# Performance work log

Measured on AMD Instinct MI355X. Metric: run time of the kernel, lower is better.

The kernel has to match this reference:

```python
import jax, jax.numpy as jnp
import numpy as np

B, H, W, C, G = 4, 56, 56, 256, 16
K = 9  # 3x3 deformable kernel
GC = C // G


def _ln(x, g, b, eps=1e-5):
    mu = jnp.mean(x, axis=-1, keepdims=True)
    var = jnp.mean(jnp.square(x - mu), axis=-1, keepdims=True)
    return (x - mu) * jax.lax.rsqrt(var + eps) * g + b


def _gelu(x):
    return jax.nn.gelu(x, approximate=False)  # torch nn.GELU default = exact erf


def _dcnv3_core(x, offset, mask):
    # x: [B,H,W,C]; offset: [B,H,W,G*K*2] (x,y per point); mask: [B,H,W,G,K] softmaxed over K
    xg = x.reshape(B, H * W, G, GC)
    off = offset.reshape(B, H, W, G, K, 2)
    dy, dx = jnp.meshgrid(jnp.arange(-1.0, 2.0), jnp.arange(-1.0, 2.0), indexing="ij")
    dx = dx.reshape(K).astype(x.dtype)
    dy = dy.reshape(K).astype(x.dtype)
    gx = jnp.arange(W, dtype=x.dtype)[None, None, :, None, None]
    gy = jnp.arange(H, dtype=x.dtype)[None, :, None, None, None]
    # sampling locations in unpadded pixel coords (zeros outside image == F.pad + zero grid_sample)
    px = gx + dx + off[..., 0]  # [B,H,W,G,K]
    py = gy + dy + off[..., 1]

    def flat(p):  # [B,H,W,G,K] -> [B, H*W*K, G]
        return p.transpose(0, 1, 2, 4, 3).reshape(B, H * W * K, G)

    pxf, pyf = flat(px), flat(py)
    x0 = jnp.floor(pxf)
    y0 = jnp.floor(pyf)
    acc = jnp.zeros((B, H * W * K, G, GC), x.dtype)
    for cx, cy in ((x0, y0), (x0 + 1, y0), (x0, y0 + 1), (x0 + 1, y0 + 1)):
        wgt = (1 - jnp.abs(pxf - cx)) * (1 - jnp.abs(pyf - cy))
        valid = ((cx >= 0) & (cx < W) & (cy >= 0) & (cy < H)).astype(x.dtype)
        idx = (jnp.clip(cy, 0, H - 1).astype(jnp.int32) * W
               + jnp.clip(cx, 0, W - 1).astype(jnp.int32))[..., None]  # [B,HWK,G,1]
        v = jnp.take_along_axis(xg, idx, axis=1)  # [B,HWK,G,GC]
        acc = acc + (wgt * valid)[..., None] * v
    mf = flat(mask)[..., None]  # [B,HWK,G,1]
    out = (acc * mf).reshape(B, H * W, K, G, GC).sum(axis=2)
    return out.reshape(B, H, W, C)


def _dcn(x, w_in, b_in, w_dw, b_dw, ln_dw_g, ln_dw_b, w_off, b_off,
         w_mask, b_mask, w_out, b_out):
    xp = x @ w_in + b_in  # input projection (value branch)
    x1 = jax.lax.conv_general_dilated(
        x, w_dw, window_strides=(1, 1), padding="SAME",
        dimension_numbers=("NHWC", "HWIO", "NHWC"), feature_group_count=C) + b_dw
    x1 = _gelu(_ln(x1, ln_dw_g, ln_dw_b))  # dw_conv -> LN -> GELU
    offset = x1 @ w_off + b_off  # [B,H,W,G*K*2]
    mask = jax.nn.softmax((x1 @ w_mask + b_mask).reshape(B, H, W, G, K), axis=-1)
    y = _dcnv3_core(xp, offset, mask)
    return y @ w_out + b_out


def _block(x, w_in, b_in, w_dw, b_dw, ln_dw_g, ln_dw_b, w_off, b_off,
           w_mask, b_mask, w_out, b_out, ln1_g, ln1_b,
           w_fc1, b_fc1, w_fc2, b_fc2, ln2_g, ln2_b, gamma1, gamma2):
    # post_norm=True: x = x + gamma1*LN1(dcn(x)); x = x + gamma2*LN2(mlp(x))
    y = _dcn(x, w_in, b_in, w_dw, b_dw, ln_dw_g, ln_dw_b, w_off, b_off,
             w_mask, b_mask, w_out, b_out)
    x = x + gamma1 * _ln(y, ln1_g, ln1_b)
    m = _gelu(x @ w_fc1 + b_fc1) @ w_fc2 + b_fc2  # MLP (dropout = identity)
    x = x + gamma2 * _ln(m, ln2_g, ln2_b)
    return x


def setup_inputs() -> dict:
    key = jax.random.key(0)
    ks = jax.random.split(key, 9)
    f = jnp.float32

    def rn(k, shape, s=0.02):
        return jax.random.normal(k, shape, dtype=f) * s

    return {
        "x": jax.random.normal(ks[0], (B, H, W, C), dtype=f),
        "w_in": rn(ks[1], (C, C)), "b_in": jnp.zeros((C,), f),
        "w_dw": rn(ks[2], (3, 3, 1, C), 0.1), "b_dw": jnp.zeros((C,), f),
        "ln_dw_g": jnp.ones((C,), f), "ln_dw_b": jnp.zeros((C,), f),
        "w_off": rn(ks[3], (C, G * K * 2)), "b_off": jnp.zeros((G * K * 2,), f),
        "w_mask": rn(ks[4], (C, G * K)), "b_mask": jnp.zeros((G * K,), f),
        "w_out": rn(ks[5], (C, C)), "b_out": jnp.zeros((C,), f),
        "ln1_g": jnp.ones((C,), f), "ln1_b": jnp.zeros((C,), f),
        "w_fc1": rn(ks[6], (C, C)), "b_fc1": jnp.zeros((C,), f),
        "w_fc2": rn(ks[7], (C, C)), "b_fc2": jnp.zeros((C,), f),
        "ln2_g": jnp.ones((C,), f), "ln2_b": jnp.zeros((C,), f),
        "gamma1": jnp.ones((C,), f), "gamma2": jnp.ones((C,), f),
    }


def reference(x, w_in, b_in, w_dw, b_dw, ln_dw_g, ln_dw_b, w_off, b_off,
              w_mask, b_mask, w_out, b_out, ln1_g, ln1_b,
              w_fc1, b_fc1, w_fc2, b_fc2, ln2_g, ln2_b, gamma1, gamma2):
    return _block(x, w_in, b_in, w_dw, b_dw, ln_dw_g, ln_dw_b, w_off, b_off,
                  w_mask, b_mask, w_out, b_out, ln1_g, ln1_b,
                  w_fc1, b_fc1, w_fc2, b_fc2, ln2_g, ln2_b, gamma1, gamma2)
```

## Files before the change

### kernel.cpp

```cpp
#include <hip/hip_runtime.h>
#include <math.h>

typedef unsigned short u16;
typedef unsigned int u32;
typedef __attribute__((ext_vector_type(8))) short short8;
typedef __attribute__((ext_vector_type(4))) float f32x4;

#define NB 4
#define NH 56
#define NW 56
#define HW2 (NH*NW)
#define NPIX (NB*HW2)

__device__ __forceinline__ u16 f2b(float f) {
  union { float f; u32 u; } a; a.f = f;
  return (u16)((a.u + 0x7FFFu + ((a.u >> 16) & 1u)) >> 16);
}
__device__ __forceinline__ float b2f(u16 v) {
  union { u32 u; float f; } a; a.u = ((u32)v) << 16; return a.f;
}
__device__ __forceinline__ float gelu_exact(float v) {
  return 0.5f * v * (1.0f + erff(v * 0.70710678118654752f));
}
__device__ __forceinline__ int xcd_swz(int bid, int nwg) {
  const int q = nwg >> 3, r = nwg & 7, x = bid & 7, j = bid >> 3;
  return (x < r ? x * (q + 1) : r * (q + 1) + (x - r) * q) + j;
}
__device__ __forceinline__ u32 swz(int r, int b) {
  return (u32)(r * 512 + ((b ^ (r & 7)) << 4));
}

__global__ __launch_bounds__(256) void k1_kernel(
    const float* __restrict__ w_in, const float* __restrict__ w_out,
    const float* __restrict__ w_fc1, const float* __restrict__ w_fc2,
    const float* __restrict__ w_off, const float* __restrict__ w_mask,
    const float* __restrict__ b_off, const float* __restrict__ b_mask,
    u16* __restrict__ wT, float* __restrict__ bias_cat,
    const float* __restrict__ xf, const float* __restrict__ wdw,
    const float* __restrict__ bdw, const float* __restrict__ lng,
    const float* __restrict__ lnb, u16* __restrict__ x1)
{
  const int blk = blockIdx.x, t = threadIdx.x;
  if (blk < 1456) {
    const float* src; int n, N;
    if      (blk < 256)  { src = w_in;   n = blk;        N = 256; }
    else if (blk < 512)  { src = w_out;  n = blk - 256;  N = 256; }
    else if (blk < 768)  { src = w_fc1;  n = blk - 512;  N = 256; }
    else if (blk < 1024) { src = w_fc2;  n = blk - 768;  N = 256; }
    else if (blk < 1312) { src = w_off;  n = blk - 1024; N = 288; }
    else                 { src = w_mask; n = blk - 1312; N = 144; }
    wT[blk * 256 + t] = f2b(src[t * N + n]);
  } else if (blk == 1456) {
    for (int j = t; j < 432; j += 256)
      bias_cat[j] = (j < 288) ? b_off[j] : b_mask[j - 288];
  } else {
    const int pb = xcd_swz(blk - 1457, 3136);
    const int p = pb * 4 + (t >> 6);
    const int lane = t & 63, c0 = lane * 4;
    const int bb = p / HW2, hw = p - bb * HW2;
    const int h = hw / NW, w = hw - h * NW;
    float4 bd = *(const float4*)(bdw + c0);
    float a0 = bd.x, a1 = bd.y, a2 = bd.z, a3 = bd.w;
    #pragma unroll
    for (int kh = 0; kh < 3; ++kh) {
      const int hh = h + kh - 1;
      if ((unsigned)hh >= NH) continue;
      #pragma unroll
      for (int kw = 0; kw < 3; ++kw) {
        const int ww = w + kw - 1;
        if ((unsigned)ww >= NW) continue;
        float4 v = *(const float4*)(xf + (size_t)(bb * HW2 + hh * NW + ww) * 256 + c0);
        float4 wv = *(const float4*)(wdw + (kh * 3 + kw) * 256 + c0);
        a0 += v.x * wv.x; a1 += v.y * wv.y;
        a2 += v.z * wv.z; a3 += v.w * wv.w;
      }
    }
    float s1 = a0 + a1 + a2 + a3;
    float s2 = a0 * a0 + a1 * a1 + a2 * a2 + a3 * a3;
    #pragma unroll
    for (int d = 1; d < 64; d <<= 1) { s1 += __shfl_xor(s1, d); s2 += __shfl_xor(s2, d); }
    const float mu = s1 * (1.0f / 256.0f);
    const float var = s2 * (1.0f / 256.0f) - mu * mu;
    const float rs = rsqrtf(var + 1e-5f);
    float4 lg4 = *(const float4*)(lng + c0);
    float4 lb4 = *(const float4*)(lnb + c0);
    ushort4 o;
    o.x = f2b(gelu_exact((a0 - mu) * rs * lg4.x + lb4.x));
    o.y = f2b(gelu_exact((a1 - mu) * rs * lg4.y + lb4.y));
    o.z = f2b(gelu_exact((a2 - mu) * rs * lg4.z + lb4.z));
    o.w = f2b(gelu_exact((a3 - mu) * rs * lg4.w + lb4.w));
    *(ushort4*)(x1 + (size_t)p * 256 + c0) = o;
  }
}

template<int AF32>
__device__ __forceinline__ void gemm64_body(
    const void* __restrict__ Asrc, const u16* __restrict__ Brows,
    const float* __restrict__ bias, u16* __restrict__ Cout,
    int Ntot, int m0, int n0, char* As, char* Bs, int t)
{
  if (AF32) {
    const int r = t >> 2;
    const float4* src = (const float4*)((const float*)Asrc + (size_t)(m0 + r) * 256);
    #pragma unroll
    for (int i = 0; i < 16; ++i) {
      const int f4 = (t & 3) + i * 4;
      float4 v = src[f4];
      uint2 pk;
      pk.x = (u32)f2b(v.x) | ((u32)f2b(v.y) << 16);
      pk.y = (u32)f2b(v.z) | ((u32)f2b(v.w) << 16);
      *(uint2*)(As + swz(r, f4 >> 1) + (f4 & 1) * 8) = pk;
    }
  } else {
    const int r = t >> 2, c0 = t & 3;
    const u16* Ag = (const u16*)Asrc + (size_t)(m0 + r) * 256;
    #pragma unroll
    for (int i = 0; i < 8; ++i) {
      const int b = c0 + i * 4;
      *(uint4*)(As + swz(r, b)) = *(const uint4*)(Ag + b * 8);
    }
  }
  {
    const int r = t >> 2, c0 = t & 3;
    const int nrow = n0 + r;
    const u16* Bg = Brows + (size_t)nrow * 256;
    const bool bok = nrow < Ntot;
    #pragma unroll
    for (int i = 0; i < 8; ++i) {
      const int b = c0 + i * 4;
      uint4 bv = make_uint4(0u, 0u, 0u, 0u);
      if (bok) bv = *(const uint4*)(Bg + b * 8);
      *(uint4*)(Bs + swz(r, b)) = bv;
    }
  }
  __syncthreads();
  const int l = t & 63, w = t >> 6;
  const int wm = (w >> 1) << 5, wn = (w & 1) << 5;
  const int lr = l & 15, lk = l >> 4;
  const int ra0 = wm + lr, ra1 = wm + 16 + lr;
  const int rb0 = wn + lr, rb1 = wn + 16 + lr;
  f32x4 acc00 = {}, acc01 = {}, acc10 = {}, acc11 = {};
  #pragma unroll
  for (int ks = 0; ks < 8; ++ks) {
    const int bb = ks * 4 + lk;
    short8 a0 = *(const short8*)(As + swz(ra0, bb));
    short8 a1 = *(const short8*)(As + swz(ra1, bb));
    short8 b0 = *(const short8*)(Bs + swz(rb0, bb));
    short8 b1 = *(const short8*)(Bs + swz(rb1, bb));
    acc00 = __builtin_amdgcn_mfma_f32_16x16x32_bf16(a0, b0, acc00, 0, 0, 0);
    acc01 = __builtin_amdgcn_mfma_f32_16x16x32_bf16(a0, b1, acc01, 0, 0, 0);
    acc10 = __builtin_amdgcn_mfma_f32_16x16x32_bf16(a1, b0, acc10, 0, 0, 0);
    acc11 = __builtin_amdgcn_mfma_f32_16x16x32_bf16(a1, b1, acc11, 0, 0, 0);
  }
  const f32x4 accs[2][2] = {{acc00, acc01}, {acc10, acc11}};
  #pragma unroll
  for (int mi = 0; mi < 2; ++mi)
    #pragma unroll
    for (int ni = 0; ni < 2; ++ni) {
      const int col = n0 + wn + ni * 16 + lr;
      if (col < Ntot) {
        const float bv = bias[col];
        #pragma unroll
        for (int r4 = 0; r4 < 4; ++r4) {
          const int row = m0 + wm + mi * 16 + lk * 4 + r4;
          Cout[(size_t)row * Ntot + col] = f2b(accs[mi][ni][r4] + bv);
        }
      }
    }
}

__global__ __launch_bounds__(256) void k2_kernel(
    const float* __restrict__ xf, const u16* __restrict__ x1,
    const u16* __restrict__ wT, const float* __restrict__ b_in,
    const float* __restrict__ bcat, u16* __restrict__ xp_bf,
    u16* __restrict__ omb)
{
  __shared__ u16 lds[32768];
  char* As = (char*)lds;
  char* Bs = (char*)(lds + 16384);
  const int t = threadIdx.x;
  if (blockIdx.x < 784) {
    const int sb = xcd_swz(blockIdx.x, 784);
    const int m0 = (sb >> 2) * 64, n0 = (sb & 3) * 64;
    gemm64_body<1>(xf, wT, b_in, xp_bf, 256, m0, n0, As, Bs, t);
  } else {
    const int sb = xcd_swz((int)blockIdx.x - 784, 1372);
    const int m0 = (sb / 7) * 64, n0 = (sb % 7) * 64;
    gemm64_body<0>(x1, wT + 1024 * 256, bcat, omb, 432, m0, n0, As, Bs, t);
  }
}

__global__ __launch_bounds__(256) void dcnv3_kernel(
    const u16* __restrict__ xp, const u16* __restrict__ omb,
    u16* __restrict__ y)
{
  __shared__ u16 lom[8 * 432];
  const int sb = xcd_swz(blockIdx.x, NPIX / 8);
  const int p0 = sb * 8;
  for (int i = threadIdx.x; i < 432; i += 256) {
    const int row = i / 54, u = i - row * 54;
    *(uint4*)(lom + row * 432 + u * 8) =
        *(const uint4*)(omb + (size_t)(p0 + row) * 432 + u * 8);
  }
  __syncthreads();
  const int tid = threadIdx.x;
  const int lp = tid >> 5, gh = tid & 31;
  const int g = gh >> 1, hf = gh & 1;
  const int p = p0 + lp;
  const int bb = p / HW2, hw = p - bb * HW2;
  const int h = hw / NW, w = hw - h * NW;
  const u16* off = lom + lp * 432 + g * 18;
  const u16* mk  = lom + lp * 432 + 288 + g * 9;
  float lg[9];
  float mx = -1e30f;
  #pragma unroll
  for (int k = 0; k < 9; ++k) { lg[k] = b2f(mk[k]); mx = fmaxf(mx, lg[k]); }
  float se = 0.0f;
  #pragma unroll
  for (int k = 0; k < 9; ++k) { lg[k] = __expf(lg[k] - mx); se += lg[k]; }
  const float inv = 1.0f / se;

  float a[8] = {0.f,0.f,0.f,0.f,0.f,0.f,0.f,0.f};
  const u16* base = xp + ((size_t)bb * HW2) * 256 + g * 16 + hf * 8;
  #pragma unroll
  for (int k = 0; k < 9; ++k) {
    const float px = (float)(w + (k % 3) - 1) + b2f(off[2 * k]);
    const float py = (float)(h + (k / 3) - 1) + b2f(off[2 * k + 1]);
    const float fx = floorf(px), fy = floorf(py);
    const int ix = (int)fx, iy = (int)fy;
    const float ax = px - fx, ay = py - fy;
    const float mwt = lg[k] * inv;
    const float w00 = (1.0f - ax) * (1.0f - ay) * mwt;
    const float w10 = ax * (1.0f - ay) * mwt;
    const float w01 = (1.0f - ax) * ay * mwt;
    const float w11 = ax * ay * mwt;
    auto corner = [&](int cx, int cy, float wt) {
      if (cx < 0 || cx >= NW || cy < 0 || cy >= NH) return;
      uint4 v = *(const uint4*)(base + (size_t)(cy * NW + cx) * 256);
      const u32 wv[4] = {v.x, v.y, v.z, v.w};
      #pragma unroll
      for (int j = 0; j < 4; ++j) {
        union { u32 u; float f; } lo, hi;
        lo.u = wv[j] << 16; hi.u = wv[j] & 0xffff0000u;
        a[2 * j]     += wt * lo.f;
        a[2 * j + 1] += wt * hi.f;
      }
    };
    corner(ix,     iy,     w00);
    corner(ix + 1, iy,     w10);
    corner(ix,     iy + 1, w01);
    corner(ix + 1, iy + 1, w11);
  }
  u16 tmp[8];
  #pragma unroll
  for (int j = 0; j < 8; ++j) tmp[j] = f2b(a[j]);
  *(uint4*)(y + ((size_t)p * 256 + g * 16 + hf * 8)) = *(const uint4*)(tmp);
}

__global__ __launch_bounds__(512) void mega3_kernel(
    const u16* __restrict__ ybf, const u16* __restrict__ wT,
    const float* __restrict__ x, const float* __restrict__ b_out,
    const float* __restrict__ gamma1, const float* __restrict__ ln1g,
    const float* __restrict__ ln1b, const float* __restrict__ b_fc1,
    const float* __restrict__ b_fc2, const float* __restrict__ gamma2,
    const float* __restrict__ ln2g, const float* __restrict__ ln2b,
    float* __restrict__ out)
{
  __shared__ u16 As[64 * 256];
  __shared__ float redS[64][4], redQ[64][4];
  const int t = threadIdx.x;
  const int m0 = blockIdx.x * 64;
  const int l = t & 63, w = t >> 6;
  const int wm = w >> 2, wn = w & 3;
  const int lr = l & 15, lk = l >> 4;
  const int ra0 = wm * 32 + lr, ra1 = wm * 32 + 16 + lr;
  const int colb = wn * 64 + lr;

  {
    const int r = t >> 3, j0 = (t & 7) * 4;
    const uint4* src = (const uint4*)(ybf + (size_t)(m0 + r) * 256);
    #pragma unroll
    for (int i = 0; i < 4; ++i)
      *(uint4*)((char*)As + swz(r, j0 + i)) = src[j0 + i];
  }
  __syncthreads();

  f32x4 acc[2][4];
  auto do_gemm = [&](const u16* Bt) {
    #pragma unroll
    for (int mi = 0; mi < 2; ++mi)
      #pragma unroll
      for (int ni = 0; ni < 4; ++ni) acc[mi][ni] = (f32x4){0.f,0.f,0.f,0.f};
    const u16* Bbase = Bt + (size_t)(wn * 64 + lr) * 256 + lk * 8;
    #pragma unroll
    for (int ks = 0; ks < 8; ++ks) {
      short8 a0 = *(const short8*)((char*)As + swz(ra0, ks * 4 + lk));
      short8 a1 = *(const short8*)((char*)As + swz(ra1, ks * 4 + lk));
      #pragma unroll
      for (int ni = 0; ni < 4; ++ni) {
        short8 b = *(const short8*)(Bbase + ni * 16 * 256 + ks * 32);
        acc[0][ni] = __builtin_amdgcn_mfma_f32_16x16x32_bf16(a0, b, acc[0][ni], 0, 0, 0);
        acc[1][ni] = __builtin_amdgcn_mfma_f32_16x16x32_bf16(a1, b, acc[1][ni], 0, 0, 0);
      }
    }
  };
  auto lds_write_b16 = [&](int row, int col, u16 v) {
    *(u16*)((char*)As + row * 512 + (((col >> 3) ^ (row & 7)) << 4) + (col & 7) * 2) = v;
  };
  auto ln_reduce = [&](const float bv[4], float s1[2][4], float s2[2][4]) {
    #pragma unroll
    for (int mi = 0; mi < 2; ++mi)
      #pragma unroll
      for (int r4 = 0; r4 < 4; ++r4) {
        float s = 0.f, q = 0.f;
        #pragma unroll
        for (int ni = 0; ni < 4; ++ni) {
          const float v = acc[mi][ni][r4] + bv[ni];
          s += v; q += v * v;
        }
        s1[mi][r4] = s; s2[mi][r4] = q;
      }
    #pragma unroll
    for (int d = 1; d < 16; d <<= 1)
      #pragma unroll
      for (int mi = 0; mi < 2; ++mi)
        #pragma unroll
        for (int r4 = 0; r4 < 4; ++r4) {
          s1[mi][r4] += __shfl_xor(s1[mi][r4], d);
          s2[mi][r4] += __shfl_xor(s2[mi][r4], d);
        }
    if (lr == 0) {
      #pragma unroll
      for (int mi = 0; mi < 2; ++mi)
        #pragma unroll
        for (int r4 = 0; r4 < 4; ++r4) {
          const int rl = wm * 32 + mi * 16 + lk * 4 + r4;
          redS[rl][wn] = s1[mi][r4];
          redQ[rl][wn] = s2[mi][r4];
        }
    }
    __syncthreads();
  };

  do_gemm(wT + 256 * 256);
  float bv1[4], s1[2][4], s2[2][4];
  #pragma unroll
  for (int ni = 0; ni < 4; ++ni) bv1[ni] = b_out[colb + ni * 16];
  ln_reduce(bv1, s1, s2);

  float x2r[2][4][4];
  {
    float gmv[4], lgv[4], lbv[4];
    #pragma unroll
    for (int ni = 0; ni < 4; ++ni) {
      gmv[ni] = gamma1[colb + ni * 16];
      lgv[ni] = ln1g[colb + ni * 16];
      lbv[ni] = ln1b[colb + ni * 16];
    }
    #pragma unroll
    for (int mi = 0; mi < 2; ++mi)
      #pragma unroll
      for (int r4 = 0; r4 < 4; ++r4) {
        const int rl = wm * 32 + mi * 16 + lk * 4 + r4;
        const float S = redS[rl][0] + redS[rl][1] + redS[rl][2] + redS[rl][3];
        const float Q = redQ[rl][0] + redQ[rl][1] + redQ[rl][2] + redQ[rl][3];
        const float mu = S * (1.0f / 256.0f);
        const float var = Q * (1.0f / 256.0f) - mu * mu;
        const float rs = rsqrtf(var + 1e-5f);
        const int row = m0 + rl;
        #pragma unroll
        for (int ni = 0; ni < 4; ++ni) {
          const float v = acc[mi][ni][r4] + bv1[ni];
          const float o = x[(size_t)row * 256 + colb + ni * 16]
                        + gmv[ni] * ((v - mu) * rs * lgv[ni] + lbv[ni]);
          x2r[mi][r4][ni] = o;
          lds_write_b16(rl, colb + ni * 16, f2b(o));
        }
      }
  }
  __syncthreads();

  do_gemm(wT + 512 * 256);
  float m1v[2][4][4];
  #pragma unroll
  for (int mi = 0; mi < 2; ++mi)
    #pragma unroll
    for (int r4 = 0; r4 < 4; ++r4)
      #pragma unroll
      for (int ni = 0; ni < 4; ++ni)
        m1v[mi][r4][ni] = gelu_exact(acc[mi][ni][r4] + b_fc1[colb + ni * 16]);
  __syncthreads();
  #pragma unroll
  for (int mi = 0; mi < 2; ++mi)
    #pragma unroll
    for (int r4 = 0; r4 < 4; ++r4) {
      const int rl = wm * 32 + mi * 16 + lk * 4 + r4;
      #pragma unroll
      for (int ni = 0; ni < 4; ++ni)
        lds_write_b16(rl, colb + ni * 16, f2b(m1v[mi][r4][ni]));
    }
  __syncthreads();

  do_gemm(wT + 768 * 256);
  float bv3[4];
  #pragma unroll
  for (int ni = 0; ni < 4; ++ni) bv3[ni] = b_fc2[colb + ni * 16];
  ln_reduce(bv3, s1, s2);
  {
    float gmv[4], lgv[4], lbv[4];
    #pragma unroll
    for (int ni = 0; ni < 4; ++ni) {
      gmv[ni] = gamma2[colb + ni * 16];
      lgv[ni] = ln2g[colb + ni * 16];
      lbv[ni] = ln2b[colb + ni * 16];
    }
    #pragma unroll
    for (int mi = 0; mi < 2; ++mi)
      #pragma unroll
      for (int r4 = 0; r4 < 4; ++r4) {
        const int rl = wm * 32 + mi * 16 + lk * 4 + r4;
        const float S = redS[rl][0] + redS[rl][1] + redS[rl][2] + redS[rl][3];
        const float Q = redQ[rl][0] + redQ[rl][1] + redQ[rl][2] + redQ[rl][3];
        const float mu = S * (1.0f / 256.0f);
        const float var = Q * (1.0f / 256.0f) - mu * mu;
        const float rs = rsqrtf(var + 1e-5f);
        const int row = m0 + rl;
        #pragma unroll
        for (int ni = 0; ni < 4; ++ni) {
          const float v = acc[mi][ni][r4] + bv3[ni];
          out[(size_t)row * 256 + colb + ni * 16] =
              x2r[mi][r4][ni] + gmv[ni] * ((v - mu) * rs * lgv[ni] + lbv[ni]);
        }
      }
  }
}

static constexpr size_t OFF_WT  = 0;
static constexpr size_t OFF_BC  = 745472;
static constexpr size_t OFF_XP  = 747520;
static constexpr size_t OFF_X1  = 7170048;
static constexpr size_t OFF_OMB = 13592576;
static constexpr size_t OFF_Y   = 24430592;

extern "C" void kernel_launch(void* const* d_in, const int* in_sizes, int n_in,
                              void* d_out, int out_size, void* d_ws, size_t ws_size,
                              hipStream_t stream)
{
  const float* x      = (const float*)d_in[0];
  const float* w_in   = (const float*)d_in[1];
  const float* b_in   = (const float*)d_in[2];
  const float* w_dw   = (const float*)d_in[3];
  const float* b_dw   = (const float*)d_in[4];
  const float* ln_dw_g= (const float*)d_in[5];
  const float* ln_dw_b= (const float*)d_in[6];
  const float* w_off  = (const float*)d_in[7];
  const float* b_off  = (const float*)d_in[8];
  const float* w_mask = (const float*)d_in[9];
  const float* b_mask = (const float*)d_in[10];
  const float* w_out  = (const float*)d_in[11];
  const float* b_out  = (const float*)d_in[12];
  const float* ln1_g  = (const float*)d_in[13];
  const float* ln1_b  = (const float*)d_in[14];
  const float* w_fc1  = (const float*)d_in[15];
  const float* b_fc1  = (const float*)d_in[16];
  const float* w_fc2  = (const float*)d_in[17];
  const float* b_fc2  = (const float*)d_in[18];
  const float* ln2_g  = (const float*)d_in[19];
  const float* ln2_b  = (const float*)d_in[20];
  const float* gamma1 = (const float*)d_in[21];
  const float* gamma2 = (const float*)d_in[22];
  float* out = (float*)d_out;

  char* ws = (char*)d_ws;
  u16*   wT    = (u16*)  (ws + OFF_WT);
  float* bcat  = (float*)(ws + OFF_BC);
  u16*   xp_bf = (u16*)  (ws + OFF_XP);
  u16*   x1    = (u16*)  (ws + OFF_X1);
  u16*   omb   = (u16*)  (ws + OFF_OMB);
  u16*   ybf   = (u16*)  (ws + OFF_Y);

  k1_kernel<<<dim3(1457 + 3136), 256, 0, stream>>>(
      w_in, w_out, w_fc1, w_fc2, w_off, w_mask, b_off, b_mask, wT, bcat,
      x, w_dw, b_dw, ln_dw_g, ln_dw_b, x1);
  k2_kernel<<<dim3(784 + 1372), 256, 0, stream>>>(
      x, x1, wT, b_in, bcat, xp_bf, omb);
  dcnv3_kernel<<<dim3(NPIX / 8), 256, 0, stream>>>(xp_bf, omb, ybf);
  mega3_kernel<<<dim3(196), 512, 0, stream>>>(
      ybf, wT, x, b_out, gamma1, ln1_g, ln1_b, b_fc1, b_fc2,
      gamma2, ln2_g, ln2_b, out);
}
```

Before: 93.46 us.

## Stage neighborhood tile of xp in LDS for deformable sampling

The DCNv3 sampling kernel now cooperatively loads a 5x12 pixel window of the value projection (all 256 channels) into shared memory around each block's 8 pixels. Bilinear corner fetches whose sample falls inside that window read from LDS, and the rest fall back to global memory. This is meant to cut repeated scattered global or L2 gathers, since neighbouring output pixels hit overlapping input texels. In exchange it adds about 30KB of LDS per block, which can lower occupancy, adds an upfront tile load that may fetch unused data, and introduces a divergent branch. It also assumes the 8 pixels of a block lie in one image row (56 is divisible by 8).

```diff
diff --git a/kernel.cpp b/kernel.cpp
--- a/kernel.cpp
+++ b/kernel.cpp
@@ -195,20 +195,32 @@
     u16* __restrict__ y)
 {
   __shared__ u16 lom[8 * 432];
+  __shared__ u16 ltile[5 * 12 * 256];
   const int sb = xcd_swz(blockIdx.x, NPIX / 8);
   const int p0 = sb * 8;
+  const int bb = p0 / HW2, hw0 = p0 - bb * HW2;
+  const int h = hw0 / NW, w0 = hw0 - h * NW;
+  const u16* xb = xp + (size_t)bb * HW2 * 256;
   for (int i = threadIdx.x; i < 432; i += 256) {
     const int row = i / 54, u = i - row * 54;
     *(uint4*)(lom + row * 432 + u * 8) =
         *(const uint4*)(omb + (size_t)(p0 + row) * 432 + u * 8);
   }
+  for (int i = threadIdx.x; i < 1920; i += 256) {
+    const int texel = i >> 5, part = i & 31;
+    const int ly = texel / 12, lx = texel - ly * 12;
+    const int gy = h - 2 + ly, gx = w0 - 2 + lx;
+    if ((unsigned)gy < NH && (unsigned)gx < NW)
+      *(uint4*)(ltile + texel * 256 + part * 8) =
+          *(const uint4*)(xb + (size_t)(gy * NW + gx) * 256 + part * 8);
+  }
   __syncthreads();
+
   const int tid = threadIdx.x;
   const int lp = tid >> 5, gh = tid & 31;
   const int g = gh >> 1, hf = gh & 1;
-  const int p = p0 + lp;
-  const int bb = p / HW2, hw = p - bb * HW2;
-  const int h = hw / NW, w = hw - h * NW;
+  const int w = w0 + lp;
+  const int choff = g * 16 + hf * 8;
   const u16* off = lom + lp * 432 + g * 18;
   const u16* mk  = lom + lp * 432 + 288 + g * 9;
   float lg[9];
@@ -221,7 +233,17 @@
   const float inv = 1.0f / se;
 
   float a[8] = {0.f,0.f,0.f,0.f,0.f,0.f,0.f,0.f};
-  const u16* base = xp + ((size_t)bb * HW2) * 256 + g * 16 + hf * 8;
+  const u16* gbase = xb + choff;
+  auto fma8 = [&](uint4 v, float wt) {
+    const u32 wv[4] = {v.x, v.y, v.z, v.w};
+    #pragma unroll
+    for (int j = 0; j < 4; ++j) {
+      union { u32 u; float f; } lo, hi;
+      lo.u = wv[j] << 16; hi.u = wv[j] & 0xffff0000u;
+      a[2 * j]     += wt * lo.f;
+      a[2 * j + 1] += wt * hi.f;
+    }
+  };
   #pragma unroll
   for (int k = 0; k < 9; ++k) {
     const float px = (float)(w + (k % 3) - 1) + b2f(off[2 * k]);
@@ -234,27 +256,32 @@
     const float w10 = ax * (1.0f - ay) * mwt;
     const float w01 = (1.0f - ax) * ay * mwt;
     const float w11 = ax * ay * mwt;
-    auto corner = [&](int cx, int cy, float wt) {
-      if (cx < 0 || cx >= NW || cy < 0 || cy >= NH) return;
-      uint4 v = *(const uint4*)(base + (size_t)(cy * NW + cx) * 256);
-      const u32 wv[4] = {v.x, v.y, v.z, v.w};
-      #pragma unroll
-      for (int j = 0; j < 4; ++j) {
-        union { u32 u; float f; } lo, hi;
-        lo.u = wv[j] << 16; hi.u = wv[j] & 0xffff0000u;
-        a[2 * j]     += wt * lo.f;
-        a[2 * j + 1] += wt * hi.f;
-      }
-    };
-    corner(ix,     iy,     w00);
-    corner(ix + 1, iy,     w10);
-    corner(ix,     iy + 1, w01);
-    corner(ix + 1, iy + 1, w11);
+    const bool inw = (ix >= w0 - 2) && (ix <= w0 + 8) && (iy >= h - 2) && (iy <= h + 1);
+    if (inw) {
+      auto cornerL = [&](int cx, int cy, float wt) {
+        if (cx < 0 || cx >= NW || cy < 0 || cy >= NH) return;
+        const u16* vp = ltile + (((cy - (h - 2)) * 12 + (cx - (w0 - 2))) << 8) + choff;
+        fma8(*(const uint4*)vp, wt);
+      };
+      cornerL(ix,     iy,     w00);
+      cornerL(ix + 1, iy,     w10);
+      cornerL(ix,     iy + 1, w01);
+      cornerL(ix + 1, iy + 1, w11);
+    } else {
+      auto cornerG = [&](int cx, int cy, float wt) {
+        if (cx < 0 || cx >= NW || cy < 0 || cy >= NH) return;
+        fma8(*(const uint4*)(gbase + (size_t)(cy * NW + cx) * 256), wt);
+      };
+      cornerG(ix,     iy,     w00);
+      cornerG(ix + 1, iy,     w10);
+      cornerG(ix,     iy + 1, w01);
+      cornerG(ix + 1, iy + 1, w11);
+    }
   }
   u16 tmp[8];
   #pragma unroll
   for (int j = 0; j < 8; ++j) tmp[j] = f2b(a[j]);
-  *(uint4*)(y + ((size_t)p * 256 + g * 16 + hf * 8)) = *(const uint4*)(tmp);
+  *(uint4*)(y + ((size_t)(p0 + lp) * 256 + choff)) = *(const uint4*)(tmp);
 }
 
 __global__ __launch_bounds__(512) void mega3_kernel(
```

Result: no change. 94.48 us (+1.1%).

## Fuse DCNv3 sampling into the output-projection/MLP tail kernel

Applied to the files above, without the earlier changes.

Merges the deformable sampling kernel into the tail GEMM+LayerNorm+MLP kernel. Each 512-thread block now handles 32 pixels, writing the sampled output straight into swizzled LDS instead of round-tripping a bf16 buffer through global memory. This also removes one kernel launch. In exchange, the tail GEMMs use 32-row tiles with 8 waves splitting N, so each loaded weight is reused less. The sampling phase also has fewer threads per pixel (16 instead of 32), each doing twice the work.

```diff
diff --git a/kernel.cpp b/kernel.cpp
--- a/kernel.cpp
+++ b/kernel.cpp
@@ -190,114 +190,100 @@
   }
 }
 
-__global__ __launch_bounds__(256) void dcnv3_kernel(
+__global__ __launch_bounds__(512) void dcn_tail_kernel(
     const u16* __restrict__ xp, const u16* __restrict__ omb,
-    u16* __restrict__ y)
+    const u16* __restrict__ wT, const float* __restrict__ x,
+    const float* __restrict__ b_out, const float* __restrict__ gamma1,
+    const float* __restrict__ ln1g, const float* __restrict__ ln1b,
+    const float* __restrict__ b_fc1, const float* __restrict__ b_fc2,
+    const float* __restrict__ gamma2, const float* __restrict__ ln2g,
+    const float* __restrict__ ln2b, float* __restrict__ out)
 {
-  __shared__ u16 lom[8 * 432];
-  const int sb = xcd_swz(blockIdx.x, NPIX / 8);
-  const int p0 = sb * 8;
-  for (int i = threadIdx.x; i < 432; i += 256) {
+  __shared__ u16 As[32 * 256];
+  __shared__ u16 lom[32 * 432];
+  __shared__ float redS[32][8], redQ[32][8];
+  const int t = threadIdx.x;
+  const int blk = xcd_swz(blockIdx.x, 392);
+  const int p0 = blk * 32;
+
+  for (int i = t; i < 1728; i += 512) {
     const int row = i / 54, u = i - row * 54;
     *(uint4*)(lom + row * 432 + u * 8) =
         *(const uint4*)(omb + (size_t)(p0 + row) * 432 + u * 8);
   }
   __syncthreads();
-  const int tid = threadIdx.x;
-  const int lp = tid >> 5, gh = tid & 31;
-  const int g = gh >> 1, hf = gh & 1;
-  const int p = p0 + lp;
-  const int bb = p / HW2, hw = p - bb * HW2;
-  const int h = hw / NW, w = hw - h * NW;
-  const u16* off = lom + lp * 432 + g * 18;
-  const u16* mk  = lom + lp * 432 + 288 + g * 9;
-  float lg[9];
-  float mx = -1e30f;
-  #pragma unroll
-  for (int k = 0; k < 9; ++k) { lg[k] = b2f(mk[k]); mx = fmaxf(mx, lg[k]); }
-  float se = 0.0f;
-  #pragma unroll
-  for (int k = 0; k < 9; ++k) { lg[k] = __expf(lg[k] - mx); se += lg[k]; }
-  const float inv = 1.0f / se;
-
-  float a[8] = {0.f,0.f,0.f,0.f,0.f,0.f,0.f,0.f};
-  const u16* base = xp + ((size_t)bb * HW2) * 256 + g * 16 + hf * 8;
-  #pragma unroll
-  for (int k = 0; k < 9; ++k) {
-    const float px = (float)(w + (k % 3) - 1) + b2f(off[2 * k]);
-    const float py = (float)(h + (k / 3) - 1) + b2f(off[2 * k + 1]);
-    const float fx = floorf(px), fy = floorf(py);
-    const int ix = (int)fx, iy = (int)fy;
-    const float ax = px - fx, ay = py - fy;
-    const float mwt = lg[k] * inv;
-    const float w00 = (1.0f - ax) * (1.0f - ay) * mwt;
-    const float w10 = ax * (1.0f - ay) * mwt;
-    const float w01 = (1.0f - ax) * ay * mwt;
-    const float w11 = ax * ay * mwt;
+
+  {
+    const int lp = t >> 4, g = t & 15;
+    const int p = p0 + lp;
+    const int bb = p / HW2, hw = p - bb * HW2;
+    const int h = hw / NW, w = hw - h * NW;
+    const u16* off = lom + lp * 432 + g * 18;
+    const u16* mk  = lom + lp * 432 + 288 + g * 9;
+    float lg[9];
+    float mx = -1e30f;
+    #pragma unroll
+    for (int k = 0; k < 9; ++k) { lg[k] = b2f(mk[k]); mx = fmaxf(mx, lg[k]); }
+    float se = 0.0f;
+    #pragma unroll
+    for (int k = 0; k < 9; ++k) { lg[k] = __expf(lg[k] - mx); se += lg[k]; }
+    const float inv = 1.0f / se;
+    float a[16];
+    #pragma unroll
+    for (int j = 0; j < 16; ++j) a[j] = 0.f;
+    const u16* gbase = xp + (size_t)bb * HW2 * 256 + g * 16;
     auto corner = [&](int cx, int cy, float wt) {
       if (cx < 0 || cx >= NW || cy < 0 || cy >= NH) return;
-      uint4 v = *(const uint4*)(base + (size_t)(cy * NW + cx) * 256);
-      const u32 wv[4] = {v.x, v.y, v.z, v.w};
-      #pragma unroll
-      for (int j = 0; j < 4; ++j) {
+      const u16* vp = gbase + (size_t)(cy * NW + cx) * 256;
+      uint4 v0 = *(const uint4*)vp;
+      uint4 v1 = *(const uint4*)(vp + 8);
+      const u32 wv[8] = {v0.x, v0.y, v0.z, v0.w, v1.x, v1.y, v1.z, v1.w};
+      #pragma unroll
+      for (int j = 0; j < 8; ++j) {
         union { u32 u; float f; } lo, hi;
         lo.u = wv[j] << 16; hi.u = wv[j] & 0xffff0000u;
         a[2 * j]     += wt * lo.f;
         a[2 * j + 1] += wt * hi.f;
       }
     };
-    corner(ix,     iy,     w00);
-    corner(ix + 1, iy,     w10);
-    corner(ix,     iy + 1, w01);
-    corner(ix + 1, iy + 1, w11);
-  }
-  u16 tmp[8];
-  #pragma unroll
-  for (int j = 0; j < 8; ++j) tmp[j] = f2b(a[j]);
-  *(uint4*)(y + ((size_t)p * 256 + g * 16 + hf * 8)) = *(const uint4*)(tmp);
-}
-
-__global__ __launch_bounds__(512) void mega3_kernel(
-    const u16* __restrict__ ybf, const u16* __restrict__ wT,
-    const float* __restrict__ x, const float* __restrict__ b_out,
-    const float* __restrict__ gamma1, const float* __restrict__ ln1g,
-    const float* __restrict__ ln1b, const float* __restrict__ b_fc1,
-    const float* __restrict__ b_fc2, const float* __restrict__ gamma2,
-    const float* __restrict__ ln2g, const float* __restrict__ ln2b,
-    float* __restrict__ out)
-{
-  __shared__ u16 As[64 * 256];
-  __shared__ float redS[64][4], redQ[64][4];
-  const int t = threadIdx.x;
-  const int m0 = blockIdx.x * 64;
-  const int l = t & 63, w = t >> 6;
-  const int wm = w >> 2, wn = w & 3;
+    #pragma unroll
+    for (int k = 0; k < 9; ++k) {
+      const float px = (float)(w + (k % 3) - 1) + b2f(off[2 * k]);
+      const float py = (float)(h + (k / 3) - 1) + b2f(off[2 * k + 1]);
+      const float fx = floorf(px), fy = floorf(py);
+      const int ix = (int)fx, iy = (int)fy;
+      const float ax = px - fx, ay = py - fy;
+      const float mwt = lg[k] * inv;
+      corner(ix,     iy,     (1.0f - ax) * (1.0f - ay) * mwt);
+      corner(ix + 1, iy,     ax * (1.0f - ay) * mwt);
+      corner(ix,     iy + 1, (1.0f - ax) * ay * mwt);
+      corner(ix + 1, iy + 1, ax * ay * mwt);
+    }
+    u16 tmp[16];
+    #pragma unroll
+    for (int j = 0; j < 16; ++j) tmp[j] = f2b(a[j]);
+    const int u0 = g * 2;
+    *(uint4*)((char*)As + lp * 512 + (((u0    ) ^ (lp & 7)) << 4)) = *(const uint4*)(tmp);
+    *(uint4*)((char*)As + lp * 512 + (((u0 + 1) ^ (lp & 7)) << 4)) = *(const uint4*)(tmp + 8);
+  }
+  __syncthreads();
+
+  const int l = t & 63, w8 = t >> 6;
   const int lr = l & 15, lk = l >> 4;
-  const int ra0 = wm * 32 + lr, ra1 = wm * 32 + 16 + lr;
-  const int colb = wn * 64 + lr;
-
-  {
-    const int r = t >> 3, j0 = (t & 7) * 4;
-    const uint4* src = (const uint4*)(ybf + (size_t)(m0 + r) * 256);
-    #pragma unroll
-    for (int i = 0; i < 4; ++i)
-      *(uint4*)((char*)As + swz(r, j0 + i)) = src[j0 + i];
-  }
-  __syncthreads();
-
-  f32x4 acc[2][4];
+  const int colb = w8 * 32 + lr;
+  f32x4 acc[2][2];
   auto do_gemm = [&](const u16* Bt) {
     #pragma unroll
     for (int mi = 0; mi < 2; ++mi)
       #pragma unroll
-      for (int ni = 0; ni < 4; ++ni) acc[mi][ni] = (f32x4){0.f,0.f,0.f,0.f};
-    const u16* Bbase = Bt + (size_t)(wn * 64 + lr) * 256 + lk * 8;
+      for (int ni = 0; ni < 2; ++ni) acc[mi][ni] = (f32x4){0.f, 0.f, 0.f, 0.f};
+    const u16* Bbase = Bt + (size_t)(w8 * 32 + lr) * 256 + lk * 8;
     #pragma unroll
     for (int ks = 0; ks < 8; ++ks) {
-      short8 a0 = *(const short8*)((char*)As + swz(ra0, ks * 4 + lk));
-      short8 a1 = *(const short8*)((char*)As + swz(ra1, ks * 4 + lk));
-      #pragma unroll
-      for (int ni = 0; ni < 4; ++ni) {
+      short8 a0 = *(const short8*)((char*)As + swz(lr,      ks * 4 + lk));
+      short8 a1 = *(const short8*)((char*)As + swz(16 + lr, ks * 4 + lk));
+      #pragma unroll
+      for (int ni = 0; ni < 2; ++ni) {
         short8 b = *(const short8*)(Bbase + ni * 16 * 256 + ks * 32);
         acc[0][ni] = __builtin_amdgcn_mfma_f32_16x16x32_bf16(a0, b, acc[0][ni], 0, 0, 0);
         acc[1][ni] = __builtin_amdgcn_mfma_f32_16x16x32_bf16(a1, b, acc[1][ni], 0, 0, 0);
@@ -307,14 +293,15 @@
   auto lds_write_b16 = [&](int row, int col, u16 v) {
     *(u16*)((char*)As + row * 512 + (((col >> 3) ^ (row & 7)) << 4) + (col & 7) * 2) = v;
   };
-  auto ln_reduce = [&](const float bv[4], float s1[2][4], float s2[2][4]) {
+  auto ln_reduce = [&](const float bv[2]) {
+    float s1[2][4], s2[2][4];
     #pragma unroll
     for (int mi = 0; mi < 2; ++mi)
       #pragma unroll
       for (int r4 = 0; r4 < 4; ++r4) {
         float s = 0.f, q = 0.f;
         #pragma unroll
-        for (int ni = 0; ni < 4; ++ni) {
+        for (int ni = 0; ni < 2; ++ni) {
           const float v = acc[mi][ni][r4] + bv[ni];
           s += v; q += v * v;
         }
@@ -334,45 +321,43 @@
       for (int mi = 0; mi < 2; ++mi)
         #pragma unroll
         for (int r4 = 0; r4 < 4; ++r4) {
-          const int rl = wm * 32 + mi * 16 + lk * 4 + r4;
-          redS[rl][wn] = s1[mi][r4];
-          redQ[rl][wn] = s2[mi][r4];
+          const int rl = mi * 16 + lk * 4 + r4;
+          redS[rl][w8] = s1[mi][r4];
+          redQ[rl][w8] = s2[mi][r4];
         }
     }
     __syncthreads();
   };
+  auto row_stats = [&](int rl, float& mu, float& rs) {
+    float S = 0.f, Q = 0.f;
+    #pragma unroll
+    for (int j = 0; j < 8; ++j) { S += redS[rl][j]; Q += redQ[rl][j]; }
+    mu = S * (1.0f / 256.0f);
+    const float var = Q * (1.0f / 256.0f) - mu * mu;
+    rs = rsqrtf(var + 1e-5f);
+  };
 
   do_gemm(wT + 256 * 256);
-  float bv1[4], s1[2][4], s2[2][4];
-  #pragma unroll
-  for (int ni = 0; ni < 4; ++ni) bv1[ni] = b_out[colb + ni * 16];
-  ln_reduce(bv1, s1, s2);
-
-  float x2r[2][4][4];
+  float bv1[2] = {b_out[colb], b_out[colb + 16]};
+  ln_reduce(bv1);
+
+  float x2r[2][4][2];
   {
-    float gmv[4], lgv[4], lbv[4];
-    #pragma unroll
-    for (int ni = 0; ni < 4; ++ni) {
-      gmv[ni] = gamma1[colb + ni * 16];
-      lgv[ni] = ln1g[colb + ni * 16];
-      lbv[ni] = ln1b[colb + ni * 16];
-    }
+    const float gm[2]  = {gamma1[colb], gamma1[colb + 16]};
+    const float lgv[2] = {ln1g[colb],   ln1g[colb + 16]};
+    const float lbv[2] = {ln1b[colb],   ln1b[colb + 16]};
     #pragma unroll
     for (int mi = 0; mi < 2; ++mi)
       #pragma unroll
       for (int r4 = 0; r4 < 4; ++r4) {
-        const int rl = wm * 32 + mi * 16 + lk * 4 + r4;
-        const float S = redS[rl][0] + redS[rl][1] + redS[rl][2] + redS[rl][3];
-        const float Q = redQ[rl][0] + redQ[rl][1] + redQ[rl][2] + redQ[rl][3];
-        const float mu = S * (1.0f / 256.0f);
-        const float var = Q * (1.0f / 256.0f) - mu * mu;
-        const float rs = rsqrtf(var + 1e-5f);
-        const int row = m0 + rl;
-        #pragma unroll
-        for (int ni = 0; ni < 4; ++ni) {
+        const int rl = mi * 16 + lk * 4 + r4;
+        float mu, rs; row_stats(rl, mu, rs);
+        const int row = p0 + rl;
+        #pragma unroll
+        for (int ni = 0; ni < 2; ++ni) {
           const float v = acc[mi][ni][r4] + bv1[ni];
           const float o = x[(size_t)row * 256 + colb + ni * 16]
-                        + gmv[ni] * ((v - mu) * rs * lgv[ni] + lbv[ni]);
+                        + gm[ni] * ((v - mu) * rs * lgv[ni] + lbv[ni]);
           x2r[mi][r4][ni] = o;
           lds_write_b16(rl, colb + ni * 16, f2b(o));
         }
@@ -381,55 +366,46 @@
   __syncthreads();
 
   do_gemm(wT + 512 * 256);
-  float m1v[2][4][4];
+  float m1v[2][4][2];
+  const float bf1[2] = {b_fc1[colb], b_fc1[colb + 16]};
   #pragma unroll
   for (int mi = 0; mi < 2; ++mi)
     #pragma unroll
     for (int r4 = 0; r4 < 4; ++r4)
       #pragma unroll
-      for (int ni = 0; ni < 4; ++ni)
-        m1v[mi][r4][ni] = gelu_exact(acc[mi][ni][r4] + b_fc1[colb + ni * 16]);
+      for (int ni = 0; ni < 2; ++ni)
+        m1v[mi][r4][ni] = gelu_exact(acc[mi][ni][r4] + bf1[ni]);
   __syncthreads();
   #pragma unroll
   for (int mi = 0; mi < 2; ++mi)
     #pragma unroll
     for (int r4 = 0; r4 < 4; ++r4) {
-      const int rl = wm * 32 + mi * 16 + lk * 4 + r4;
-      #pragma unroll
-      for (int ni = 0; ni < 4; ++ni)
+      const int rl = mi * 16 + lk * 4 + r4;
+      #pragma unroll
+      for (int ni = 0; ni < 2; ++ni)
         lds_write_b16(rl, colb + ni * 16, f2b(m1v[mi][r4][ni]));
     }
   __syncthreads();
 
   do_gemm(wT + 768 * 256);
-  float bv3[4];
-  #pragma unroll
-  for (int ni = 0; ni < 4; ++ni) bv3[ni] = b_fc2[colb + ni * 16];
-  ln_reduce(bv3, s1, s2);
+  float bv3[2] = {b_fc2[colb], b_fc2[colb + 16]};
+  ln_reduce(bv3);
   {
-    float gmv[4], lgv[4], lbv[4];
-    #pragma unroll
-    for (int ni = 0; ni < 4; ++ni) {
-      gmv[ni] = gamma2[colb + ni * 16];
-      lgv[ni] = ln2g[colb + ni * 16];
-      lbv[ni] = ln2b[colb + ni * 16];
-    }
+    const float gm[2]  = {gamma2[colb], gamma2[colb + 16]};
+    const float lgv[2] = {ln2g[colb],   ln2g[colb + 16]};
+    const float lbv[2] = {ln2b[colb],   ln2b[colb + 16]};
     #pragma unroll
     for (int mi = 0; mi < 2; ++mi)
       #pragma unroll
       for (int r4 = 0; r4 < 4; ++r4) {
-        const int rl = wm * 32 + mi * 16 + lk * 4 + r4;
-        const float S = redS[rl][0] + redS[rl][1] + redS[rl][2] + redS[rl][3];
-        const float Q = redQ[rl][0] + redQ[rl][1] + redQ[rl][2] + redQ[rl][3];
-        const float mu = S * (1.0f / 256.0f);
-        const float var = Q * (1.0f / 256.0f) - mu * mu;
-        const float rs = rsqrtf(var + 1e-5f);
-        const int row = m0 + rl;
-        #pragma unroll
-        for (int ni = 0; ni < 4; ++ni) {
+        const int rl = mi * 16 + lk * 4 + r4;
+        float mu, rs; row_stats(rl, mu, rs);
+        const int row = p0 + rl;
+        #pragma unroll
+        for (int ni = 0; ni < 2; ++ni) {
           const float v = acc[mi][ni][r4] + bv3[ni];
           out[(size_t)row * 256 + colb + ni * 16] =
-              x2r[mi][r4][ni] + gmv[ni] * ((v - mu) * rs * lgv[ni] + lbv[ni]);
+              x2r[mi][r4][ni] + gm[ni] * ((v - mu) * rs * lgv[ni] + lbv[ni]);
         }
       }
   }
@@ -440,7 +416,6 @@
 static constexpr size_t OFF_XP  = 747520;
 static constexpr size_t OFF_X1  = 7170048;
 static constexpr size_t OFF_OMB = 13592576;
-static constexpr size_t OFF_Y   = 24430592;
 
 extern "C" void kernel_launch(void* const* d_in, const int* in_sizes, int n_in,
                               void* d_out, int out_size, void* d_ws, size_t ws_size,
@@ -477,15 +452,13 @@
   u16*   xp_bf = (u16*)  (ws + OFF_XP);
   u16*   x1    = (u16*)  (ws + OFF_X1);
   u16*   omb   = (u16*)  (ws + OFF_OMB);
-  u16*   ybf   = (u16*)  (ws + OFF_Y);
 
   k1_kernel<<<dim3(1457 + 3136), 256, 0, stream>>>(
       w_in, w_out, w_fc1, w_fc2, w_off, w_mask, b_off, b_mask, wT, bcat,
       x, w_dw, b_dw, ln_dw_g, ln_dw_b, x1);
   k2_kernel<<<dim3(784 + 1372), 256, 0, stream>>>(
       x, x1, wT, b_in, bcat, xp_bf, omb);
-  dcnv3_kernel<<<dim3(NPIX / 8), 256, 0, stream>>>(xp_bf, omb, ybf);
-  mega3_kernel<<<dim3(196), 512, 0, stream>>>(
-      ybf, wT, x, b_out, gamma1, ln1_g, ln1_b, b_fc1, b_fc2,
+  dcn_tail_kernel<<<dim3(392), 512, 0, stream>>>(
+      xp_bf, omb, wT, x, b_out, gamma1, ln1_g, ln1_b, b_fc1, b_fc2,
       gamma2, ln2_g, ln2_b, out);
 }
```

Measured after the change: 88.09 us, median of 2. 1.06x faster.
